# Performance work log

Hardware: AMD Instinct MI355X
Metric: run time of the kernel (lower is better)

## Reference

```python
import jax, jax.numpy as jnp
import numpy as np

B, C, T, H, K = 512, 64, 512, 128, 16
EPS_BN = 1e-5


def setup_inputs() -> dict:
    key = jax.random.key(0)
    ks = jax.random.split(key, 8)
    s = 0.05
    return {
        "x": jax.random.normal(ks[0], (B, C, T), jnp.float32),
        "conv1_w": jax.random.normal(ks[1], (H, C, 3), jnp.float32) * s,
        "conv1_b": jnp.zeros((H,), jnp.float32),
        "conv2_w": jax.random.normal(ks[2], (H, H, 3), jnp.float32) * s,
        "conv2_b": jnp.zeros((H,), jnp.float32),
        "bnt1_g": jnp.ones((H,), jnp.float32), "bnt1_b": jnp.zeros((H,), jnp.float32),
        "bnt2_g": jnp.ones((H,), jnp.float32), "bnt2_b": jnp.zeros((H,), jnp.float32),
        "W1": jax.random.normal(ks[3], (T, H), jnp.float32) * s, "b1": jnp.zeros((H,), jnp.float32),
        "g1": jnp.ones((H,), jnp.float32), "be1": jnp.zeros((H,), jnp.float32),
        "W2": jax.random.normal(ks[4], (H, H), jnp.float32) * s, "b2": jnp.zeros((H,), jnp.float32),
        "g2": jnp.ones((H,), jnp.float32), "be2": jnp.zeros((H,), jnp.float32),
        "W3": jax.random.normal(ks[5], (H, H), jnp.float32) * s, "b3": jnp.zeros((H,), jnp.float32),
        "g3": jnp.ones((H,), jnp.float32), "be3": jnp.zeros((H,), jnp.float32),
    }


def _bn_nc(z, g, b):
    # BatchNorm1d on (N, C) with batch statistics (training-mode normalization)
    m = z.mean(0)
    v = z.var(0)
    return (z - m) * jax.lax.rsqrt(v + EPS_BN) * g + b


def _bn_ncl(z, g, b):
    # BatchNorm1d on (N, C, L)
    m = z.mean((0, 2), keepdims=True)
    v = z.var((0, 2), keepdims=True)
    return (z - m) * jax.lax.rsqrt(v + EPS_BN) * g[None, :, None] + b[None, :, None]


def _conv1d(z, w, b):
    y = jax.lax.conv_general_dilated(z, w, (1,), "SAME",
                                     dimension_numbers=("NCH", "OIH", "NCH"))
    return y + b[None, :, None]


def _forward(x, conv1_w, conv1_b, conv2_w, conv2_b, bnt1_g, bnt1_b, bnt2_g, bnt2_b,
             W1, b1, g1, be1, W2, b2, g2, be2, W3, b3, g3, be3):
    # temporal branch: computed but unused in the output (faithful to the source)
    ht = jax.nn.relu(_bn_ncl(_conv1d(x, conv1_w, conv1_b), bnt1_g, bnt1_b))
    ht = jax.nn.relu(_bn_ncl(_conv1d(ht, conv2_w, conv2_b), bnt2_g, bnt2_b))

    # dynamic graph: cosine similarity averaged over batch, top-k neighbors per channel
    xn = x / jnp.maximum(jnp.linalg.norm(x, axis=2, keepdims=True), 1e-12)
    sim = jnp.einsum("bct,bdt->cd", xn, xn) / x.shape[0]  # (C, C)
    _, nbr = jax.lax.top_k(sim, K)                        # (C, K)
    src = jnp.repeat(jnp.arange(C), K)                    # (C*K,)
    dst = nbr.reshape(-1)                                 # (C*K,)
    offs = (jnp.arange(B) * C)[:, None]
    N = B * C
    sl = jnp.arange(N)
    # edge_index[0]=source node i, edge_index[1]=its top-k neighbor; plus GCN self-loops
    es = jnp.concatenate([(src[None, :] + offs).reshape(-1), sl])
    ed = jnp.concatenate([(dst[None, :] + offs).reshape(-1), sl])

    deg = jax.ops.segment_sum(jnp.ones(es.shape[0], x.dtype), ed, num_segments=N)
    dinv = jax.lax.rsqrt(deg)  # deg >= 1 due to self-loops
    enorm = dinv[es] * dinv[ed]

    def gcn(h, W, b):
        hw = h @ W
        return jax.ops.segment_sum(hw[es] * enorm[:, None], ed, num_segments=N) + b

    # source does permute(0,2,1).view(B*C, T): a flat reshape of the (B, T, C) tensor
    nodes = jnp.transpose(x, (0, 2, 1)).reshape(N, T)
    h = jax.nn.relu(_bn_nc(gcn(nodes, W1, b1), g1, be1))
    h = jax.nn.relu(_bn_nc(gcn(h, W2, b2), g2, be2))
    h = jax.nn.relu(_bn_nc(gcn(h, W3, b3), g3, be3))
    return h.reshape(B, C * H)


def reference(x, conv1_w, conv1_b, conv2_w, conv2_b, bnt1_g, bnt1_b, bnt2_g, bnt2_b,
              W1, b1, g1, be1, W2, b2, g2, be2, W3, b3, g3, be3):
    return _forward(x, conv1_w, conv1_b, conv2_w, conv2_b, bnt1_g, bnt1_b,
                    bnt2_g, bnt2_b, W1, b1, g1, be1, W2, b2, g2, be2,
                    W3, b3, g3, be3)
```

## Files before the change

### kernel.cpp

```cpp
#include <hip/hip_runtime.h>
#include <math.h>

#define B_  512
#define C_  64
#define T_  512
#define H_  128
#define N_  (B_*C_)

typedef unsigned int   uint_;
typedef unsigned short ushort_;
typedef unsigned long long ull_;

typedef __attribute__((ext_vector_type(8))) short bf8v;
typedef __attribute__((ext_vector_type(4))) float f4v;

#define OFF_SIMP   0u
#define OFF_Z2     0u
#define OFF_Z1     8388608u
#define OFF_Z3     16777216u
#define OFF_WT1    25165824u
#define OFF_WT2    25296896u
#define OFF_WT3    25329664u
#define OFF_MASKS  25362432u
#define OFF_MB     25395200u
#define OFF_SS1    25403392u
#define OFF_SS2    25404416u
#define OFF_SS3    25405440u
#define OFF_BNPART 25406464u
#define OFF_BNP2   25930752u

__device__ __forceinline__ ushort_ f2bf(float f) {
    uint_ u = __float_as_uint(f);
    u = (u + 0x7FFFu + ((u >> 16) & 1u)) >> 16;
    return (ushort_)u;
}
__device__ __forceinline__ float bf2f(ushort_ s) {
    return __uint_as_float(((uint_)s) << 16);
}

__global__ __launch_bounds__(256) void k_gram(const float* __restrict__ x,
                                              float* __restrict__ simpart)
{
    __shared__ ushort_ Xh[64 * 136];
    __shared__ ushort_ Xl[64 * 136];
    __shared__ float  gd[64];
    __shared__ double rn[64];

    const int b = blockIdx.x;
    const int t = threadIdx.x;
    const int w = t >> 6, l = t & 63;
    const int lr = l & 15, lg = l >> 4;
    const int r0 = (w >> 1) * 2, c0 = (w & 1) * 2;

    f4v acc[2][2];
#pragma unroll
    for (int i = 0; i < 2; ++i)
#pragma unroll
        for (int j = 0; j < 2; ++j) acc[i][j] = (f4v)0.f;

    const float* xb = x + (size_t)b * (C_ * T_);

    for (int j = 0; j < 4; ++j) {
#pragma unroll
        for (int it = 0; it < 8; ++it) {
            int i = t + 256 * it;
            int c = i >> 5, t4 = i & 31;
            float4 v = *(const float4*)&xb[(size_t)c * T_ + 128 * j + 4 * t4];
            ushort_ h0 = f2bf(v.x), h1 = f2bf(v.y), h2 = f2bf(v.z), h3 = f2bf(v.w);
            uint2 ph;
            ph.x = (uint_)h0 | ((uint_)h1 << 16);
            ph.y = (uint_)h2 | ((uint_)h3 << 16);
            float e0 = v.x - bf2f(h0), e1 = v.y - bf2f(h1);
            float e2 = v.z - bf2f(h2), e3 = v.w - bf2f(h3);
            uint2 pl;
            pl.x = (uint_)f2bf(e0) | ((uint_)f2bf(e1) << 16);
            pl.y = (uint_)f2bf(e2) | ((uint_)f2bf(e3) << 16);
            *(uint2*)&Xh[c * 136 + 4 * t4] = ph;
            *(uint2*)&Xl[c * 136 + 4 * t4] = pl;
        }
        __syncthreads();

#pragma unroll
        for (int s = 0; s < 4; ++s) {
            bf8v ah[2], al[2], bh[2], bl[2];
#pragma unroll
            for (int i = 0; i < 2; ++i) {
                ah[i] = *(const bf8v*)&Xh[(16 * (r0 + i) + lr) * 136 + 32 * s + 8 * lg];
                al[i] = *(const bf8v*)&Xl[(16 * (r0 + i) + lr) * 136 + 32 * s + 8 * lg];
                bh[i] = *(const bf8v*)&Xh[(16 * (c0 + i) + lr) * 136 + 32 * s + 8 * lg];
                bl[i] = *(const bf8v*)&Xl[(16 * (c0 + i) + lr) * 136 + 32 * s + 8 * lg];
            }
#pragma unroll
            for (int i = 0; i < 2; ++i)
#pragma unroll
                for (int jj = 0; jj < 2; ++jj) {
                    acc[i][jj] = __builtin_amdgcn_mfma_f32_16x16x32_bf16(ah[i], bh[jj], acc[i][jj], 0, 0, 0);
                    acc[i][jj] = __builtin_amdgcn_mfma_f32_16x16x32_bf16(ah[i], bl[jj], acc[i][jj], 0, 0, 0);
                    acc[i][jj] = __builtin_amdgcn_mfma_f32_16x16x32_bf16(al[i], bh[jj], acc[i][jj], 0, 0, 0);
                }
        }
        __syncthreads();
    }

    if (r0 == c0) {
#pragma unroll
        for (int d = 0; d < 2; ++d)
            if (lg == (lr >> 2)) gd[16 * (r0 + d) + lr] = acc[d][d][lr & 3];
    }
    __syncthreads();
    if (t < 64) rn[t] = 1.0 / fmax(sqrt((double)gd[t]), 1e-12);
    __syncthreads();

    float* sp = simpart + (size_t)b * 4096;
#pragma unroll
    for (int i = 0; i < 2; ++i)
#pragma unroll
        for (int jj = 0; jj < 2; ++jj)
#pragma unroll
            for (int reg = 0; reg < 4; ++reg) {
                int rc = 16 * (r0 + i) + 4 * lg + reg;
                int cc = 16 * (c0 + jj) + lr;
                sp[rc * 64 + cc] = (float)((double)acc[i][jj][reg] * rn[rc] * rn[cc]);
            }
}

__global__ __launch_bounds__(256) void k_simrank(const float* __restrict__ simpart,
                                                 ull_* __restrict__ masks)
{
    __shared__ double part[4][64];
    __shared__ double sd[64];
    const int c = blockIdx.x;
    const int t = threadIdx.x;
    const int d = t & 63, g = t >> 6;

    double a = 0.0;
    const float* sp = simpart + (size_t)c * 64 + d;
    for (int i = 0; i < 128; ++i)
        a += (double)sp[(size_t)(g + 4 * i) * 4096];
    part[g][d] = a;
    __syncthreads();

    if (t < 64) {
        double s = ((part[0][t] + part[1][t]) + part[2][t]) + part[3][t];
        sd[t] = s;
        int rank = 0;
#pragma unroll
        for (int dp = 0; dp < 64; ++dp) {
            double w = sd[dp];
            rank += (w > s || (w == s && dp < t)) ? 1 : 0;
        }
        ull_ m = __ballot(rank < 16);
        if (t == 0) masks[c] = m;
    }
}

__global__ __launch_bounds__(256) void k_mkM(const ull_* __restrict__ masks,
                                             ushort_* __restrict__ Mbout)
{
    __shared__ ull_  nbrm[64];
    __shared__ float dv[64];
    const int t = threadIdx.x;

    if (t < 64) {
        ull_ mask = masks[t];
        nbrm[t] = mask;
        int deg = 1;
#pragma unroll
        for (int d = 0; d < 64; ++d) {
            ull_ bal = __ballot((int)((mask >> d) & 1ull));
            if (t == d) deg += (int)__popcll(bal);
        }
        dv[t] = 1.0f / sqrtf((float)deg);
    }
    __syncthreads();

    const int d = t >> 2, q = t & 3;
    const float dvd = dv[d];
    uint_ buf[8];
#pragma unroll
    for (int p = 0; p < 8; ++p) {
        int c0 = 16 * q + 2 * p, c1 = c0 + 1;
        float w0 = (float)((int)((nbrm[c0] >> d) & 1ull) + (c0 == d ? 1 : 0));
        float w1 = (float)((int)((nbrm[c1] >> d) & 1ull) + (c1 == d ? 1 : 0));
        buf[p] = (uint_)f2bf(w0 * dv[c0] * dvd) |
                 ((uint_)f2bf(w1 * dv[c1] * dvd) << 16);
    }
    ushort_* dst = Mbout + d * 64 + 16 * q;
    uint4 v0 = {buf[0], buf[1], buf[2], buf[3]};
    uint4 v1 = {buf[4], buf[5], buf[6], buf[7]};
    *(uint4*)&dst[0] = v0;
    *(uint4*)&dst[8] = v1;
}

__global__ __launch_bounds__(256) void k_prepw(const float* __restrict__ W1,
    const float* __restrict__ W2, const float* __restrict__ W3,
    ushort_* __restrict__ Wt1, ushort_* __restrict__ Wt2, ushort_* __restrict__ Wt3)
{
    __shared__ float L[64 * 132];
    const int blk = blockIdx.x, t = threadIdx.x;

    if (blk < 8) {
        for (int it = 0; it < 8; ++it) {
            int i = t + 256 * it;
            int ri = i >> 5, f4 = i & 31;
            int m = ri >> 3, cr = ri & 7;
            *(float4*)&L[ri * 132 + 4 * f4] =
                *(const float4*)&W1[(size_t)(64 * m + 8 * blk + cr) * H_ + 4 * f4];
        }
        __syncthreads();
        int f = t >> 1, half = t & 1;
        uint_ buf[16];
#pragma unroll
        for (int jj = 0; jj < 16; ++jj) {
            int k0 = 32 * half + 2 * jj;
            int c0 = k0 >> 3, m0 = k0 & 7;
            int c1 = (k0 + 1) >> 3, m1 = (k0 + 1) & 7;
            buf[jj] = (uint_)f2bf(L[(m0 * 8 + c0) * 132 + f]) |
                      ((uint_)f2bf(L[(m1 * 8 + c1) * 132 + f]) << 16);
        }
        ushort_* dst = Wt1 + (size_t)f * 512 + 64 * blk + 32 * half;
#pragma unroll
        for (int q = 0; q < 4; ++q) {
            uint4 vv = {buf[4 * q], buf[4 * q + 1], buf[4 * q + 2], buf[4 * q + 3]};
            *(uint4*)&dst[8 * q] = vv;
        }
    } else {
        const float* W = (blk < 10) ? W2 : W3;
        ushort_*     O = (blk < 10) ? Wt2 : Wt3;
        int kb = (blk - 8) & 1;
        for (int it = 0; it < 8; ++it) {
            int i = t + 256 * it;
            int ri = i >> 5, f4 = i & 31;
            *(float4*)&L[ri * 132 + 4 * f4] =
                *(const float4*)&W[(size_t)(64 * kb + ri) * H_ + 4 * f4];
        }
        __syncthreads();
        int f = t >> 1, half = t & 1;
        uint_ buf[16];
#pragma unroll
        for (int jj = 0; jj < 16; ++jj) {
            int k0 = 32 * half + 2 * jj;
            buf[jj] = (uint_)f2bf(L[k0 * 132 + f]) |
                      ((uint_)f2bf(L[(k0 + 1) * 132 + f]) << 16);
        }
        ushort_* dst = O + (size_t)f * 128 + 64 * kb + 32 * half;
#pragma unroll
        for (int q = 0; q < 4; ++q) {
            uint4 vv = {buf[4 * q], buf[4 * q + 1], buf[4 * q + 2], buf[4 * q + 3]};
            *(uint4*)&dst[8 * q] = vv;
        }
    }
}

__device__ __forceinline__ void mfma_epilogue(char* smem, int b, int t,
    f4v acc[8], const float* __restrict__ bias, const ushort_* __restrict__ Mb,
    ushort_* __restrict__ Zout, float* __restrict__ bnpart)
{
    const int l = t & 63, w = t >> 6;
    const int lr = l & 15, lg = l >> 4;

    ushort_* Yt  = (ushort_*)smem;
    ushort_* Ml  = (ushort_*)(smem + 22528);
    ushort_* Zst = (ushort_*)(smem + 33792);

#pragma unroll
    for (int nt = 0; nt < 8; ++nt) {
        uint2 p;
        p.x = (uint_)f2bf(acc[nt][0]) | ((uint_)f2bf(acc[nt][1]) << 16);
        p.y = (uint_)f2bf(acc[nt][2]) | ((uint_)f2bf(acc[nt][3]) << 16);
        *(uint2*)&Yt[(16 * nt + lr) * 88 + 16 * w + 4 * lg] = p;
    }
#pragma unroll
    for (int it = 0; it < 2; ++it) {
        int i = t + 256 * it;
        int d = i >> 3, seg = i & 7;
        *(uint4*)&Ml[d * 88 + 8 * seg] = *(const uint4*)&Mb[d * 64 + 8 * seg];
    }
    __syncthreads();

    f4v z[8];
#pragma unroll
    for (int nt = 0; nt < 8; ++nt) z[nt] = (f4v)0.f;
#pragma unroll
    for (int cs = 0; cs < 2; ++cs) {
        bf8v mf = *(const bf8v*)&Ml[(16 * w + lr) * 88 + 32 * cs + 8 * lg];
#pragma unroll
        for (int nt = 0; nt < 8; ++nt) {
            bf8v yf = *(const bf8v*)&Yt[(16 * nt + lr) * 88 + 32 * cs + 8 * lg];
            z[nt] = __builtin_amdgcn_mfma_f32_16x16x32_bf16(mf, yf, z[nt], 0, 0, 0);
        }
    }

#pragma unroll
    for (int nt = 0; nt < 8; ++nt) {
        float bv = bias[16 * nt + lr];
#pragma unroll
        for (int reg = 0; reg < 4; ++reg)
            Zst[(16 * w + 4 * lg + reg) * 136 + 16 * nt + lr] = f2bf(z[nt][reg] + bv);
    }
    __syncthreads();

    if (t < 128) {
        float s = 0.f, s2 = 0.f;
        for (int r = 0; r < 64; ++r) {
            float v = bf2f(Zst[r * 136 + t]);
            s += v; s2 += v * v;
        }
        bnpart[b * 256 + t]       = s;
        bnpart[b * 256 + 128 + t] = s2;
    }
#pragma unroll
    for (int it = 0; it < 4; ++it) {
        int i = t + 256 * it;
        int r = i >> 4, seg = i & 15;
        *(uint4*)&Zout[((size_t)(b * 64 + r)) * 128 + 8 * seg] =
            *(const uint4*)&Zst[r * 136 + 8 * seg];
    }
}

__global__ __launch_bounds__(256) void k_mgemm1(const float* __restrict__ x,
    const ushort_* __restrict__ Wt, const float* __restrict__ bias,
    const ushort_* __restrict__ Mb, ushort_* __restrict__ Zout,
    float* __restrict__ bnpart)
{
    __shared__ __align__(16) char smem[51456];
    ushort_* Al = (ushort_*)smem;
    ushort_* Wl = (ushort_*)(smem + 16640);

    const int b = blockIdx.x;
    const int t = threadIdx.x;
    const int l = t & 63, w = t >> 6;
    const int lr = l & 15, lg = l >> 4;

    f4v acc[8];
#pragma unroll
    for (int nt = 0; nt < 8; ++nt) acc[nt] = (f4v)0.f;

    const float* xb = x + (size_t)b * (C_ * T_);

    for (int j = 0; j < 4; ++j) {
#pragma unroll
        for (int it = 0; it < 8; ++it) {
            int i = t + 256 * it;
            int cr = i >> 7, t4 = i & 127;
            float4 v = *(const float4*)&xb[(size_t)(16 * j + cr) * T_ + 4 * t4];
            uint2 p;
            p.x = (uint_)f2bf(v.x) | ((uint_)f2bf(v.y) << 16);
            p.y = (uint_)f2bf(v.z) | ((uint_)f2bf(v.w) << 16);
            *(uint2*)&Al[cr * 520 + 4 * t4] = p;
        }
#pragma unroll
        for (int it = 0; it < 8; ++it) {
            int i = t + 256 * it;
            int f = i >> 4, seg = i & 15;
            *(uint4*)&Wl[f * 136 + 8 * seg] =
                *(const uint4*)&Wt[(size_t)f * 512 + 128 * j + 8 * seg];
        }
        __syncthreads();
#pragma unroll
        for (int s = 0; s < 4; ++s) {
            bf8v af = *(const bf8v*)&Al[(4 * s + lg) * 520 + 128 * w + 8 * lr];
#pragma unroll
            for (int nt = 0; nt < 8; ++nt) {
                bf8v bfv = *(const bf8v*)&Wl[(16 * nt + lr) * 136 + 32 * s + 8 * lg];
                acc[nt] = __builtin_amdgcn_mfma_f32_16x16x32_bf16(af, bfv, acc[nt], 0, 0, 0);
            }
        }
        __syncthreads();
    }
    mfma_epilogue(smem, b, t, acc, bias, Mb, Zout, bnpart);
}

__global__ __launch_bounds__(256) void k_mgemm23(const ushort_* __restrict__ Zin,
    const float* __restrict__ ss, const ushort_* __restrict__ Wt,
    const float* __restrict__ bias, const ushort_* __restrict__ Mb,
    ushort_* __restrict__ Zout, float* __restrict__ bnpart)
{
    __shared__ __align__(16) char smem[52224];
    __shared__ float ssL[256];
    ushort_* Al = (ushort_*)smem;
    ushort_* Wl = (ushort_*)(smem + 17408);

    const int b = blockIdx.x;
    const int t = threadIdx.x;
    const int l = t & 63, w = t >> 6;
    const int lr = l & 15, lg = l >> 4;

    ssL[t] = ss[t];
    __syncthreads();

    f4v acc[8];
#pragma unroll
    for (int nt = 0; nt < 8; ++nt) acc[nt] = (f4v)0.f;

#pragma unroll
    for (int it = 0; it < 4; ++it) {
        int i = t + 256 * it;
        int r = i >> 4, seg = i & 15;
        uint4 v = *(const uint4*)&Zin[((size_t)(b * 64 + r)) * 128 + 8 * seg];
        uint_ w0[4] = {v.x, v.y, v.z, v.w};
        uint_ o[4];
#pragma unroll
        for (int p = 0; p < 4; ++p) {
            int f0 = 8 * seg + 2 * p;
            float z0 = bf2f((ushort_)(w0[p] & 0xFFFF));
            float z1 = bf2f((ushort_)(w0[p] >> 16));
            float h0 = fmaxf(fmaf(z0, ssL[f0],     ssL[128 + f0]),     0.f);
            float h1 = fmaxf(fmaf(z1, ssL[f0 + 1], ssL[128 + f0 + 1]), 0.f);
            o[p] = (uint_)f2bf(h0) | ((uint_)f2bf(h1) << 16);
        }
        uint4 ov = {o[0], o[1], o[2], o[3]};
        *(uint4*)&Al[r * 136 + 8 * seg] = ov;
    }
#pragma unroll
    for (int it = 0; it < 8; ++it) {
        int i = t + 256 * it;
        int f = i >> 4, seg = i & 15;
        *(uint4*)&Wl[f * 136 + 8 * seg] =
            *(const uint4*)&Wt[(size_t)f * 128 + 8 * seg];
    }
    __syncthreads();
#pragma unroll
    for (int s = 0; s < 4; ++s) {
        bf8v af = *(const bf8v*)&Al[(16 * w + lr) * 136 + 32 * s + 8 * lg];
#pragma unroll
        for (int nt = 0; nt < 8; ++nt) {
            bf8v bfv = *(const bf8v*)&Wl[(16 * nt + lr) * 136 + 32 * s + 8 * lg];
            acc[nt] = __builtin_amdgcn_mfma_f32_16x16x32_bf16(af, bfv, acc[nt], 0, 0, 0);
        }
    }
    __syncthreads();
    mfma_epilogue(smem, b, t, acc, bias, Mb, Zout, bnpart);
}

__global__ __launch_bounds__(256) void k_bnA(const float* __restrict__ bnpart,
                                             double* __restrict__ bnp2)
{
    const int t = threadIdx.x, g = blockIdx.x;
    double a = 0.0;
    for (int i = 0; i < 16; ++i)
        a += (double)bnpart[(size_t)(16 * g + i) * 256 + t];
    bnp2[(size_t)g * 256 + t] = a;
}

__global__ __launch_bounds__(256) void k_bnB(const double* __restrict__ bnp2,
    const float* __restrict__ g, const float* __restrict__ be, float* __restrict__ ss)
{
    __shared__ double sums[256];
    const int t = threadIdx.x;
    double a = 0.0;
    for (int q = 0; q < 32; ++q) a += bnp2[(size_t)q * 256 + t];
    sums[t] = a;
    __syncthreads();
    if (t < 128) {
        double s = sums[t], s2 = sums[128 + t];
        double mean = s * (1.0 / 32768.0);
        double var  = s2 * (1.0 / 32768.0) - mean * mean;
        double rstd = 1.0 / sqrt(var + 1e-5);
        float sc = (float)((double)g[t] * rstd);
        ss[t]       = sc;
        ss[128 + t] = (float)((double)be[t] - mean * (double)sc);
    }
}

__global__ __launch_bounds__(256) void k_out(const ushort_* __restrict__ Z,
    const float* __restrict__ ss, float* __restrict__ out)
{
    int i = blockIdx.x * 256 + threadIdx.x;
    int n = i >> 4, seg = i & 15;
    uint4 v = *(const uint4*)&Z[(size_t)n * 128 + 8 * seg];
    float4 sc0 = *(const float4*)&ss[8 * seg];
    float4 sc1 = *(const float4*)&ss[8 * seg + 4];
    float4 sh0 = *(const float4*)&ss[128 + 8 * seg];
    float4 sh1 = *(const float4*)&ss[128 + 8 * seg + 4];
    uint_ wv[4] = {v.x, v.y, v.z, v.w};
    float zz[8];
#pragma unroll
    for (int p = 0; p < 4; ++p) {
        zz[2 * p]     = bf2f((ushort_)(wv[p] & 0xFFFF));
        zz[2 * p + 1] = bf2f((ushort_)(wv[p] >> 16));
    }
    float4 o0, o1;
    o0.x = fmaxf(fmaf(zz[0], sc0.x, sh0.x), 0.f);
    o0.y = fmaxf(fmaf(zz[1], sc0.y, sh0.y), 0.f);
    o0.z = fmaxf(fmaf(zz[2], sc0.z, sh0.z), 0.f);
    o0.w = fmaxf(fmaf(zz[3], sc0.w, sh0.w), 0.f);
    o1.x = fmaxf(fmaf(zz[4], sc1.x, sh1.x), 0.f);
    o1.y = fmaxf(fmaf(zz[5], sc1.y, sh1.y), 0.f);
    o1.z = fmaxf(fmaf(zz[6], sc1.z, sh1.z), 0.f);
    o1.w = fmaxf(fmaf(zz[7], sc1.w, sh1.w), 0.f);
    *(float4*)&out[(size_t)n * 128 + 8 * seg]     = o0;
    *(float4*)&out[(size_t)n * 128 + 8 * seg + 4] = o1;
}

extern "C" void kernel_launch(void* const* d_in, const int* in_sizes, int n_in,
                              void* d_out, int out_size, void* d_ws, size_t ws_size,
                              hipStream_t stream)
{
    (void)in_sizes; (void)n_in; (void)out_size; (void)ws_size;

    const float* x   = (const float*)d_in[0];
    const float* W1  = (const float*)d_in[9];
    const float* b1  = (const float*)d_in[10];
    const float* g1  = (const float*)d_in[11];
    const float* be1 = (const float*)d_in[12];
    const float* W2  = (const float*)d_in[13];
    const float* b2  = (const float*)d_in[14];
    const float* g2  = (const float*)d_in[15];
    const float* be2 = (const float*)d_in[16];
    const float* W3  = (const float*)d_in[17];
    const float* b3  = (const float*)d_in[18];
    const float* g3  = (const float*)d_in[19];
    const float* be3 = (const float*)d_in[20];

    char* ws = (char*)d_ws;
    float*   simp   = (float*)(ws + OFF_SIMP);
    ull_*    masks  = (ull_*)(ws + OFF_MASKS);
    ushort_* Mb     = (ushort_*)(ws + OFF_MB);
    ushort_* Wt1    = (ushort_*)(ws + OFF_WT1);
    ushort_* Wt2    = (ushort_*)(ws + OFF_WT2);
    ushort_* Wt3    = (ushort_*)(ws + OFF_WT3);
    float*   ss1    = (float*)(ws + OFF_SS1);
    float*   ss2    = (float*)(ws + OFF_SS2);
    float*   ss3    = (float*)(ws + OFF_SS3);
    float*   bnpart = (float*)(ws + OFF_BNPART);
    double*  bnp2   = (double*)(ws + OFF_BNP2);
    ushort_* Z1     = (ushort_*)(ws + OFF_Z1);
    ushort_* Z2     = (ushort_*)(ws + OFF_Z2);
    ushort_* Z3     = (ushort_*)(ws + OFF_Z3);
    float*   out    = (float*)d_out;

    k_prepw<<<dim3(12), dim3(256), 0, stream>>>(W1, W2, W3, Wt1, Wt2, Wt3);
    k_gram<<<dim3(512), dim3(256), 0, stream>>>(x, simp);
    k_simrank<<<dim3(64), dim3(256), 0, stream>>>(simp, masks);
    k_mkM<<<dim3(1), dim3(256), 0, stream>>>(masks, Mb);

    k_mgemm1<<<dim3(512), dim3(256), 0, stream>>>(x, Wt1, b1, Mb, Z1, bnpart);
    k_bnA<<<dim3(32), dim3(256), 0, stream>>>(bnpart, bnp2);
    k_bnB<<<dim3(1), dim3(256), 0, stream>>>(bnp2, g1, be1, ss1);

    k_mgemm23<<<dim3(512), dim3(256), 0, stream>>>(Z1, ss1, Wt2, b2, Mb, Z2, bnpart);
    k_bnA<<<dim3(32), dim3(256), 0, stream>>>(bnpart, bnp2);
    k_bnB<<<dim3(1), dim3(256), 0, stream>>>(bnp2, g2, be2, ss2);

    k_mgemm23<<<dim3(512), dim3(256), 0, stream>>>(Z2, ss2, Wt3, b3, Mb, Z3, bnpart);
    k_bnA<<<dim3(32), dim3(256), 0, stream>>>(bnpart, bnp2);
    k_bnB<<<dim3(1), dim3(256), 0, stream>>>(bnp2, g3, be3, ss3);

    k_out<<<dim3(2048), dim3(256), 0, stream>>>(Z3, ss3, out);
}
```

Baseline: 107.1 us.

## Fold tiny setup kernels into neighbors to cut launch count

Merges weight preparation into the Gram kernel as extra blocks, and drops the single-block adjacency-matrix kernel by having each GEMM block rebuild the normalized adjacency from the masks. It also removes the BN finalize kernels by having every consumer block re-reduce the 32 partial sums and compute scale/shift itself. This removes five serial launches and their tail gaps, at the cost of redundant per-block reduction and mask work and more shared memory per block.

```diff
diff --git a/kernel.cpp b/kernel.cpp
--- a/kernel.cpp
+++ b/kernel.cpp
@@ -22,10 +22,6 @@
 #define OFF_WT2    25296896u
 #define OFF_WT3    25329664u
 #define OFF_MASKS  25362432u
-#define OFF_MB     25395200u
-#define OFF_SS1    25403392u
-#define OFF_SS2    25404416u
-#define OFF_SS3    25405440u
 #define OFF_BNPART 25406464u
 #define OFF_BNP2   25930752u
 
@@ -38,90 +34,182 @@
     return __uint_as_float(((uint_)s) << 16);
 }
 
-__global__ __launch_bounds__(256) void k_gram(const float* __restrict__ x,
-                                              float* __restrict__ simpart)
-{
-    __shared__ ushort_ Xh[64 * 136];
-    __shared__ ushort_ Xl[64 * 136];
+__device__ __forceinline__ void m_preamble_wave0(const ull_* __restrict__ masks,
+                                                 ull_* nbrmS, float* dvS, int t)
+{
+    if (t < 64) {
+        ull_ mask = masks[t];
+        nbrmS[t] = mask;
+        int deg = 1;
+#pragma unroll
+        for (int d = 0; d < 64; ++d) {
+            ull_ bal = __ballot((int)((mask >> d) & 1ull));
+            if (t == d) deg += (int)__popcll(bal);
+        }
+        dvS[t] = 1.0f / sqrtf((float)deg);
+    }
+}
+
+__device__ __forceinline__ void m_build(const ull_* nbrmS, const float* dvS,
+                                        int t, uint_ m8[8])
+{
+    const int d = t >> 2, q = t & 3;
+    const float dvd = dvS[d];
+#pragma unroll
+    for (int p = 0; p < 8; ++p) {
+        int c0 = 16 * q + 2 * p, c1 = c0 + 1;
+        float w0 = (float)((int)((nbrmS[c0] >> d) & 1ull) + (c0 == d ? 1 : 0));
+        float w1 = (float)((int)((nbrmS[c1] >> d) & 1ull) + (c1 == d ? 1 : 0));
+        m8[p] = (uint_)f2bf(w0 * dvS[c0] * dvd) |
+                ((uint_)f2bf(w1 * dvS[c1] * dvd) << 16);
+    }
+}
+
+__global__ __launch_bounds__(256) void k_gramw(const float* __restrict__ x,
+    float* __restrict__ simpart,
+    const float* __restrict__ W1, const float* __restrict__ W2,
+    const float* __restrict__ W3,
+    ushort_* __restrict__ Wt1, ushort_* __restrict__ Wt2, ushort_* __restrict__ Wt3)
+{
+    __shared__ __align__(16) char smem[35584];
     __shared__ float  gd[64];
     __shared__ double rn[64];
-
-    const int b = blockIdx.x;
+    const int blk = blockIdx.x;
     const int t = threadIdx.x;
-    const int w = t >> 6, l = t & 63;
-    const int lr = l & 15, lg = l >> 4;
-    const int r0 = (w >> 1) * 2, c0 = (w & 1) * 2;
-
-    f4v acc[2][2];
-#pragma unroll
-    for (int i = 0; i < 2; ++i)
-#pragma unroll
-        for (int j = 0; j < 2; ++j) acc[i][j] = (f4v)0.f;
-
-    const float* xb = x + (size_t)b * (C_ * T_);
-
-    for (int j = 0; j < 4; ++j) {
-#pragma unroll
-        for (int it = 0; it < 8; ++it) {
-            int i = t + 256 * it;
-            int c = i >> 5, t4 = i & 31;
-            float4 v = *(const float4*)&xb[(size_t)c * T_ + 128 * j + 4 * t4];
-            ushort_ h0 = f2bf(v.x), h1 = f2bf(v.y), h2 = f2bf(v.z), h3 = f2bf(v.w);
-            uint2 ph;
-            ph.x = (uint_)h0 | ((uint_)h1 << 16);
-            ph.y = (uint_)h2 | ((uint_)h3 << 16);
-            float e0 = v.x - bf2f(h0), e1 = v.y - bf2f(h1);
-            float e2 = v.z - bf2f(h2), e3 = v.w - bf2f(h3);
-            uint2 pl;
-            pl.x = (uint_)f2bf(e0) | ((uint_)f2bf(e1) << 16);
-            pl.y = (uint_)f2bf(e2) | ((uint_)f2bf(e3) << 16);
-            *(uint2*)&Xh[c * 136 + 4 * t4] = ph;
-            *(uint2*)&Xl[c * 136 + 4 * t4] = pl;
+
+    if (blk < 512) {
+        ushort_* Xh = (ushort_*)smem;
+        ushort_* Xl = (ushort_*)(smem + 17408);
+        const int b = blk;
+        const int w = t >> 6, l = t & 63;
+        const int lr = l & 15, lg = l >> 4;
+        const int r0 = (w >> 1) * 2, c0 = (w & 1) * 2;
+
+        f4v acc[2][2];
+#pragma unroll
+        for (int i = 0; i < 2; ++i)
+#pragma unroll
+            for (int j = 0; j < 2; ++j) acc[i][j] = (f4v)0.f;
+
+        const float* xb = x + (size_t)b * (C_ * T_);
+
+        for (int j = 0; j < 4; ++j) {
+#pragma unroll
+            for (int it = 0; it < 8; ++it) {
+                int i = t + 256 * it;
+                int c = i >> 5, t4 = i & 31;
+                float4 v = *(const float4*)&xb[(size_t)c * T_ + 128 * j + 4 * t4];
+                ushort_ h0 = f2bf(v.x), h1 = f2bf(v.y), h2 = f2bf(v.z), h3 = f2bf(v.w);
+                uint2 ph;
+                ph.x = (uint_)h0 | ((uint_)h1 << 16);
+                ph.y = (uint_)h2 | ((uint_)h3 << 16);
+                float e0 = v.x - bf2f(h0), e1 = v.y - bf2f(h1);
+                float e2 = v.z - bf2f(h2), e3 = v.w - bf2f(h3);
+                uint2 pl;
+                pl.x = (uint_)f2bf(e0) | ((uint_)f2bf(e1) << 16);
+                pl.y = (uint_)f2bf(e2) | ((uint_)f2bf(e3) << 16);
+                *(uint2*)&Xh[c * 136 + 4 * t4] = ph;
+                *(uint2*)&Xl[c * 136 + 4 * t4] = pl;
+            }
+            __syncthreads();
+
+#pragma unroll
+            for (int s = 0; s < 4; ++s) {
+                bf8v ah[2], al[2], bh[2], bl[2];
+#pragma unroll
+                for (int i = 0; i < 2; ++i) {
+                    ah[i] = *(const bf8v*)&Xh[(16 * (r0 + i) + lr) * 136 + 32 * s + 8 * lg];
+                    al[i] = *(const bf8v*)&Xl[(16 * (r0 + i) + lr) * 136 + 32 * s + 8 * lg];
+                    bh[i] = *(const bf8v*)&Xh[(16 * (c0 + i) + lr) * 136 + 32 * s + 8 * lg];
+                    bl[i] = *(const bf8v*)&Xl[(16 * (c0 + i) + lr) * 136 + 32 * s + 8 * lg];
+                }
+#pragma unroll
+                for (int i = 0; i < 2; ++i)
+#pragma unroll
+                    for (int jj = 0; jj < 2; ++jj) {
+                        acc[i][jj] = __builtin_amdgcn_mfma_f32_16x16x32_bf16(ah[i], bh[jj], acc[i][jj], 0, 0, 0);
+                        acc[i][jj] = __builtin_amdgcn_mfma_f32_16x16x32_bf16(ah[i], bl[jj], acc[i][jj], 0, 0, 0);
+                        acc[i][jj] = __builtin_amdgcn_mfma_f32_16x16x32_bf16(al[i], bh[jj], acc[i][jj], 0, 0, 0);
+                    }
+            }
+            __syncthreads();
+        }
+
+        if (r0 == c0) {
+#pragma unroll
+            for (int d = 0; d < 2; ++d)
+                if (lg == (lr >> 2)) gd[16 * (r0 + d) + lr] = acc[d][d][lr & 3];
         }
         __syncthreads();
-
-#pragma unroll
-        for (int s = 0; s < 4; ++s) {
-            bf8v ah[2], al[2], bh[2], bl[2];
-#pragma unroll
-            for (int i = 0; i < 2; ++i) {
-                ah[i] = *(const bf8v*)&Xh[(16 * (r0 + i) + lr) * 136 + 32 * s + 8 * lg];
-                al[i] = *(const bf8v*)&Xl[(16 * (r0 + i) + lr) * 136 + 32 * s + 8 * lg];
-                bh[i] = *(const bf8v*)&Xh[(16 * (c0 + i) + lr) * 136 + 32 * s + 8 * lg];
-                bl[i] = *(const bf8v*)&Xl[(16 * (c0 + i) + lr) * 136 + 32 * s + 8 * lg];
-            }
-#pragma unroll
-            for (int i = 0; i < 2; ++i)
-#pragma unroll
-                for (int jj = 0; jj < 2; ++jj) {
-                    acc[i][jj] = __builtin_amdgcn_mfma_f32_16x16x32_bf16(ah[i], bh[jj], acc[i][jj], 0, 0, 0);
-                    acc[i][jj] = __builtin_amdgcn_mfma_f32_16x16x32_bf16(ah[i], bl[jj], acc[i][jj], 0, 0, 0);
-                    acc[i][jj] = __builtin_amdgcn_mfma_f32_16x16x32_bf16(al[i], bh[jj], acc[i][jj], 0, 0, 0);
+        if (t < 64) rn[t] = 1.0 / fmax(sqrt((double)gd[t]), 1e-12);
+        __syncthreads();
+
+        float* sp = simpart + (size_t)b * 4096;
+#pragma unroll
+        for (int i = 0; i < 2; ++i)
+#pragma unroll
+            for (int jj = 0; jj < 2; ++jj)
+#pragma unroll
+                for (int reg = 0; reg < 4; ++reg) {
+                    int rc = 16 * (r0 + i) + 4 * lg + reg;
+                    int cc = 16 * (c0 + jj) + lr;
+                    sp[rc * 64 + cc] = (float)((double)acc[i][jj][reg] * rn[rc] * rn[cc]);
                 }
-        }
-        __syncthreads();
-    }
-
-    if (r0 == c0) {
-#pragma unroll
-        for (int d = 0; d < 2; ++d)
-            if (lg == (lr >> 2)) gd[16 * (r0 + d) + lr] = acc[d][d][lr & 3];
-    }
-    __syncthreads();
-    if (t < 64) rn[t] = 1.0 / fmax(sqrt((double)gd[t]), 1e-12);
-    __syncthreads();
-
-    float* sp = simpart + (size_t)b * 4096;
-#pragma unroll
-    for (int i = 0; i < 2; ++i)
-#pragma unroll
-        for (int jj = 0; jj < 2; ++jj)
-#pragma unroll
-            for (int reg = 0; reg < 4; ++reg) {
-                int rc = 16 * (r0 + i) + 4 * lg + reg;
-                int cc = 16 * (c0 + jj) + lr;
-                sp[rc * 64 + cc] = (float)((double)acc[i][jj][reg] * rn[rc] * rn[cc]);
-            }
+    } else {
+        float* L = (float*)smem;
+        const int pblk = blk - 512;
+        if (pblk < 8) {
+            for (int it = 0; it < 8; ++it) {
+                int i = t + 256 * it;
+                int ri = i >> 5, f4 = i & 31;
+                int m = ri >> 3, cr = ri & 7;
+                *(float4*)&L[ri * 132 + 4 * f4] =
+                    *(const float4*)&W1[(size_t)(64 * m + 8 * pblk + cr) * H_ + 4 * f4];
+            }
+            __syncthreads();
+            int f = t >> 1, half = t & 1;
+            uint_ buf[16];
+#pragma unroll
+            for (int jj = 0; jj < 16; ++jj) {
+                int k0 = 32 * half + 2 * jj;
+                int c0 = k0 >> 3, m0 = k0 & 7;
+                int c1 = (k0 + 1) >> 3, m1 = (k0 + 1) & 7;
+                buf[jj] = (uint_)f2bf(L[(m0 * 8 + c0) * 132 + f]) |
+                          ((uint_)f2bf(L[(m1 * 8 + c1) * 132 + f]) << 16);
+            }
+            ushort_* dst = Wt1 + (size_t)f * 512 + 64 * pblk + 32 * half;
+#pragma unroll
+            for (int q = 0; q < 4; ++q) {
+                uint4 vv = {buf[4 * q], buf[4 * q + 1], buf[4 * q + 2], buf[4 * q + 3]};
+                *(uint4*)&dst[8 * q] = vv;
+            }
+        } else {
+            const float* W = (pblk < 10) ? W2 : W3;
+            ushort_*     O = (pblk < 10) ? Wt2 : Wt3;
+            int kb = (pblk - 8) & 1;
+            for (int it = 0; it < 8; ++it) {
+                int i = t + 256 * it;
+                int ri = i >> 5, f4 = i & 31;
+                *(float4*)&L[ri * 132 + 4 * f4] =
+                    *(const float4*)&W[(size_t)(64 * kb + ri) * H_ + 4 * f4];
+            }
+            __syncthreads();
+            int f = t >> 1, half = t & 1;
+            uint_ buf[16];
+#pragma unroll
+            for (int jj = 0; jj < 16; ++jj) {
+                int k0 = 32 * half + 2 * jj;
+                buf[jj] = (uint_)f2bf(L[k0 * 132 + f]) |
+                          ((uint_)f2bf(L[(k0 + 1) * 132 + f]) << 16);
+            }
+            ushort_* dst = O + (size_t)f * 128 + 64 * kb + 32 * half;
+#pragma unroll
+            for (int q = 0; q < 4; ++q) {
+                uint4 vv = {buf[4 * q], buf[4 * q + 1], buf[4 * q + 2], buf[4 * q + 3]};
+                *(uint4*)&dst[8 * q] = vv;
+            }
+        }
+    }
 }
 
 __global__ __launch_bounds__(256) void k_simrank(const float* __restrict__ simpart,
@@ -154,106 +242,8 @@
     }
 }
 
-__global__ __launch_bounds__(256) void k_mkM(const ull_* __restrict__ masks,
-                                             ushort_* __restrict__ Mbout)
-{
-    __shared__ ull_  nbrm[64];
-    __shared__ float dv[64];
-    const int t = threadIdx.x;
-
-    if (t < 64) {
-        ull_ mask = masks[t];
-        nbrm[t] = mask;
-        int deg = 1;
-#pragma unroll
-        for (int d = 0; d < 64; ++d) {
-            ull_ bal = __ballot((int)((mask >> d) & 1ull));
-            if (t == d) deg += (int)__popcll(bal);
-        }
-        dv[t] = 1.0f / sqrtf((float)deg);
-    }
-    __syncthreads();
-
-    const int d = t >> 2, q = t & 3;
-    const float dvd = dv[d];
-    uint_ buf[8];
-#pragma unroll
-    for (int p = 0; p < 8; ++p) {
-        int c0 = 16 * q + 2 * p, c1 = c0 + 1;
-        float w0 = (float)((int)((nbrm[c0] >> d) & 1ull) + (c0 == d ? 1 : 0));
-        float w1 = (float)((int)((nbrm[c1] >> d) & 1ull) + (c1 == d ? 1 : 0));
-        buf[p] = (uint_)f2bf(w0 * dv[c0] * dvd) |
-                 ((uint_)f2bf(w1 * dv[c1] * dvd) << 16);
-    }
-    ushort_* dst = Mbout + d * 64 + 16 * q;
-    uint4 v0 = {buf[0], buf[1], buf[2], buf[3]};
-    uint4 v1 = {buf[4], buf[5], buf[6], buf[7]};
-    *(uint4*)&dst[0] = v0;
-    *(uint4*)&dst[8] = v1;
-}
-
-__global__ __launch_bounds__(256) void k_prepw(const float* __restrict__ W1,
-    const float* __restrict__ W2, const float* __restrict__ W3,
-    ushort_* __restrict__ Wt1, ushort_* __restrict__ Wt2, ushort_* __restrict__ Wt3)
-{
-    __shared__ float L[64 * 132];
-    const int blk = blockIdx.x, t = threadIdx.x;
-
-    if (blk < 8) {
-        for (int it = 0; it < 8; ++it) {
-            int i = t + 256 * it;
-            int ri = i >> 5, f4 = i & 31;
-            int m = ri >> 3, cr = ri & 7;
-            *(float4*)&L[ri * 132 + 4 * f4] =
-                *(const float4*)&W1[(size_t)(64 * m + 8 * blk + cr) * H_ + 4 * f4];
-        }
-        __syncthreads();
-        int f = t >> 1, half = t & 1;
-        uint_ buf[16];
-#pragma unroll
-        for (int jj = 0; jj < 16; ++jj) {
-            int k0 = 32 * half + 2 * jj;
-            int c0 = k0 >> 3, m0 = k0 & 7;
-            int c1 = (k0 + 1) >> 3, m1 = (k0 + 1) & 7;
-            buf[jj] = (uint_)f2bf(L[(m0 * 8 + c0) * 132 + f]) |
-                      ((uint_)f2bf(L[(m1 * 8 + c1) * 132 + f]) << 16);
-        }
-        ushort_* dst = Wt1 + (size_t)f * 512 + 64 * blk + 32 * half;
-#pragma unroll
-        for (int q = 0; q < 4; ++q) {
-            uint4 vv = {buf[4 * q], buf[4 * q + 1], buf[4 * q + 2], buf[4 * q + 3]};
-            *(uint4*)&dst[8 * q] = vv;
-        }
-    } else {
-        const float* W = (blk < 10) ? W2 : W3;
-        ushort_*     O = (blk < 10) ? Wt2 : Wt3;
-        int kb = (blk - 8) & 1;
-        for (int it = 0; it < 8; ++it) {
-            int i = t + 256 * it;
-            int ri = i >> 5, f4 = i & 31;
-            *(float4*)&L[ri * 132 + 4 * f4] =
-                *(const float4*)&W[(size_t)(64 * kb + ri) * H_ + 4 * f4];
-        }
-        __syncthreads();
-        int f = t >> 1, half = t & 1;
-        uint_ buf[16];
-#pragma unroll
-        for (int jj = 0; jj < 16; ++jj) {
-            int k0 = 32 * half + 2 * jj;
-            buf[jj] = (uint_)f2bf(L[k0 * 132 + f]) |
-                      ((uint_)f2bf(L[(k0 + 1) * 132 + f]) << 16);
-        }
-        ushort_* dst = O + (size_t)f * 128 + 64 * kb + 32 * half;
-#pragma unroll
-        for (int q = 0; q < 4; ++q) {
-            uint4 vv = {buf[4 * q], buf[4 * q + 1], buf[4 * q + 2], buf[4 * q + 3]};
-            *(uint4*)&dst[8 * q] = vv;
-        }
-    }
-}
-
 __device__ __forceinline__ void mfma_epilogue(char* smem, int b, int t,
-    f4v acc[8], const float* __restrict__ bias, const ushort_* __restrict__ Mb,
+    f4v acc[8], const float* __restrict__ bias, const uint_ m8[8],
     ushort_* __restrict__ Zout, float* __restrict__ bnpart)
 {
     const int l = t & 63, w = t >> 6;
@@ -270,11 +260,12 @@
         p.y = (uint_)f2bf(acc[nt][2]) | ((uint_)f2bf(acc[nt][3]) << 16);
         *(uint2*)&Yt[(16 * nt + lr) * 88 + 16 * w + 4 * lg] = p;
     }
-#pragma unroll
-    for (int it = 0; it < 2; ++it) {
-        int i = t + 256 * it;
-        int d = i >> 3, seg = i & 7;
-        *(uint4*)&Ml[d * 88 + 8 * seg] = *(const uint4*)&Mb[d * 64 + 8 * seg];
+    {
+        const int d = t >> 2, q = t & 3;
+        uint4 v0 = {m8[0], m8[1], m8[2], m8[3]};
+        uint4 v1 = {m8[4], m8[5], m8[6], m8[7]};
+        *(uint4*)&Ml[d * 88 + 16 * q]     = v0;
+        *(uint4*)&Ml[d * 88 + 16 * q + 8] = v1;
     }
     __syncthreads();
 
@@ -320,10 +311,12 @@
 
 __global__ __launch_bounds__(256) void k_mgemm1(const float* __restrict__ x,
     const ushort_* __restrict__ Wt, const float* __restrict__ bias,
-    const ushort_* __restrict__ Mb, ushort_* __restrict__ Zout,
+    const ull_* __restrict__ masks, ushort_* __restrict__ Zout,
     float* __restrict__ bnpart)
 {
     __shared__ __align__(16) char smem[51456];
+    __shared__ ull_  nbrmS[64];
+    __shared__ float dvS[64];
     ushort_* Al = (ushort_*)smem;
     ushort_* Wl = (ushort_*)(smem + 16640);
 
@@ -331,6 +324,8 @@
     const int t = threadIdx.x;
     const int l = t & 63, w = t >> 6;
     const int lr = l & 15, lg = l >> 4;
+
+    m_preamble_wave0(masks, nbrmS, dvS, t);
 
     f4v acc[8];
 #pragma unroll
@@ -368,16 +363,22 @@
         }
         __syncthreads();
     }
-    mfma_epilogue(smem, b, t, acc, bias, Mb, Zout, bnpart);
+
+    uint_ m8[8];
+    m_build(nbrmS, dvS, t, m8);
+    mfma_epilogue(smem, b, t, acc, bias, m8, Zout, bnpart);
 }
 
 __global__ __launch_bounds__(256) void k_mgemm23(const ushort_* __restrict__ Zin,
-    const float* __restrict__ ss, const ushort_* __restrict__ Wt,
-    const float* __restrict__ bias, const ushort_* __restrict__ Mb,
+    const double* __restrict__ bnp2, const float* __restrict__ g,
+    const float* __restrict__ be, const ushort_* __restrict__ Wt,
+    const float* __restrict__ bias, const ull_* __restrict__ masks,
     ushort_* __restrict__ Zout, float* __restrict__ bnpart)
 {
     __shared__ __align__(16) char smem[52224];
     __shared__ float ssL[256];
+    __shared__ ull_  nbrmS[64];
+    __shared__ float dvS[64];
     ushort_* Al = (ushort_*)smem;
     ushort_* Wl = (ushort_*)(smem + 17408);
 
@@ -386,8 +387,24 @@
     const int l = t & 63, w = t >> 6;
     const int lr = l & 15, lg = l >> 4;
 
-    ssL[t] = ss[t];
-    __syncthreads();
+    {
+        double* sumsL = (double*)smem;
+        double a = 0.0;
+        for (int q = 0; q < 32; ++q) a += bnp2[(size_t)q * 256 + t];
+        sumsL[t] = a;
+        m_preamble_wave0(masks, nbrmS, dvS, t);
+        __syncthreads();
+        if (t < 128) {
+            double s = sumsL[t], s2 = sumsL[128 + t];
+            double mean = s * (1.0 / 32768.0);
+            double var  = s2 * (1.0 / 32768.0) - mean * mean;
+            double rstd = 1.0 / sqrt(var + 1e-5);
+            float sc = (float)((double)g[t] * rstd);
+            ssL[t]       = sc;
+            ssL[128 + t] = (float)((double)be[t] - mean * (double)sc);
+        }
+        __syncthreads();
+    }
 
     f4v acc[8];
 #pragma unroll
@@ -430,7 +447,10 @@
         }
     }
     __syncthreads();
-    mfma_epilogue(smem, b, t, acc, bias, Mb, Zout, bnpart);
+
+    uint_ m8[8];
+    m_build(nbrmS, dvS, t, m8);
+    mfma_epilogue(smem, b, t, acc, bias, m8, Zout, bnpart);
 }
 
 __global__ __launch_bounds__(256) void k_bnA(const float* __restrict__ bnpart,
@@ -443,54 +463,49 @@
     bnp2[(size_t)g * 256 + t] = a;
 }
 
-__global__ __launch_bounds__(256) void k_bnB(const double* __restrict__ bnp2,
-    const float* __restrict__ g, const float* __restrict__ be, float* __restrict__ ss)
-{
-    __shared__ double sums[256];
+__global__ __launch_bounds__(256) void k_out(const ushort_* __restrict__ Z,
+    const double* __restrict__ bnp2, const float* __restrict__ g,
+    const float* __restrict__ be, float* __restrict__ out)
+{
+    __shared__ double sumsL[256];
+    __shared__ float  ssL[256];
+    const int b = blockIdx.x;
     const int t = threadIdx.x;
+
     double a = 0.0;
     for (int q = 0; q < 32; ++q) a += bnp2[(size_t)q * 256 + t];
-    sums[t] = a;
+    sumsL[t] = a;
     __syncthreads();
     if (t < 128) {
-        double s = sums[t], s2 = sums[128 + t];
+        double s = sumsL[t], s2 = sumsL[128 + t];
         double mean = s * (1.0 / 32768.0);
         double var  = s2 * (1.0 / 32768.0) - mean * mean;
         double rstd = 1.0 / sqrt(var + 1e-5);
         float sc = (float)((double)g[t] * rstd);
-        ss[t]       = sc;
-        ss[128 + t] = (float)((double)be[t] - mean * (double)sc);
-    }
-}
-
-__global__ __launch_bounds__(256) void k_out(const ushort_* __restrict__ Z,
-    const float* __restrict__ ss, float* __restrict__ out)
-{
-    int i = blockIdx.x * 256 + threadIdx.x;
-    int n = i >> 4, seg = i & 15;
-    uint4 v = *(const uint4*)&Z[(size_t)n * 128 + 8 * seg];
-    float4 sc0 = *(const float4*)&ss[8 * seg];
-    float4 sc1 = *(const float4*)&ss[8 * seg + 4];
-    float4 sh0 = *(const float4*)&ss[128 + 8 * seg];
-    float4 sh1 = *(const float4*)&ss[128 + 8 * seg + 4];
-    uint_ wv[4] = {v.x, v.y, v.z, v.w};
-    float zz[8];
-#pragma unroll
-    for (int p = 0; p < 4; ++p) {
-        zz[2 * p]     = bf2f((ushort_)(wv[p] & 0xFFFF));
-        zz[2 * p + 1] = bf2f((ushort_)(wv[p] >> 16));
-    }
-    float4 o0, o1;
-    o0.x = fmaxf(fmaf(zz[0], sc0.x, sh0.x), 0.f);
-    o0.y = fmaxf(fmaf(zz[1], sc0.y, sh0.y), 0.f);
-    o0.z = fmaxf(fmaf(zz[2], sc0.z, sh0.z), 0.f);
-    o0.w = fmaxf(fmaf(zz[3], sc0.w, sh0.w), 0.f);
-    o1.x = fmaxf(fmaf(zz[4], sc1.x, sh1.x), 0.f);
-    o1.y = fmaxf(fmaf(zz[5], sc1.y, sh1.y), 0.f);
-    o1.z = fmaxf(fmaf(zz[6], sc1.z, sh1.z), 0.f);
-    o1.w = fmaxf(fmaf(zz[7], sc1.w, sh1.w), 0.f);
-    *(float4*)&out[(size_t)n * 128 + 8 * seg]     = o0;
-    *(float4*)&out[(size_t)n * 128 + 8 * seg + 4] = o1;
+        ssL[t]       = sc;
+        ssL[128 + t] = (float)((double)be[t] - mean * (double)sc);
+    }
+    __syncthreads();
+
+    const size_t base = (size_t)b * 64 * 128;
+#pragma unroll
+    for (int it = 0; it < 8; ++it) {
+        int i = t + 256 * it;
+        int r = i >> 5, s = i & 31;
+        uint2 v = *(const uint2*)&Z[base + (size_t)r * 128 + 4 * s];
+        float4 sc = *(const float4*)&ssL[4 * s];
+        float4 sh = *(const float4*)&ssL[128 + 4 * s];
+        float z0 = bf2f((ushort_)(v.x & 0xFFFF));
+        float z1 = bf2f((ushort_)(v.x >> 16));
+        float z2 = bf2f((ushort_)(v.y & 0xFFFF));
+        float z3 = bf2f((ushort_)(v.y >> 16));
+        float4 o;
+        o.x = fmaxf(fmaf(z0, sc.x, sh.x), 0.f);
+        o.y = fmaxf(fmaf(z1, sc.y, sh.y), 0.f);
+        o.z = fmaxf(fmaf(z2, sc.z, sh.z), 0.f);
+        o.w = fmaxf(fmaf(z3, sc.w, sh.w), 0.f);
+        *(float4*)&out[base + (size_t)r * 128 + 4 * s] = o;
+    }
 }
 
 extern "C" void kernel_launch(void* const* d_in, const int* in_sizes, int n_in,
@@ -516,13 +531,9 @@
     char* ws = (char*)d_ws;
     float*   simp   = (float*)(ws + OFF_SIMP);
     ull_*    masks  = (ull_*)(ws + OFF_MASKS);
-    ushort_* Mb     = (ushort_*)(ws + OFF_MB);
     ushort_* Wt1    = (ushort_*)(ws + OFF_WT1);
     ushort_* Wt2    = (ushort_*)(ws + OFF_WT2);
     ushort_* Wt3    = (ushort_*)(ws + OFF_WT3);
-    float*   ss1    = (float*)(ws + OFF_SS1);
-    float*   ss2    = (float*)(ws + OFF_SS2);
-    float*   ss3    = (float*)(ws + OFF_SS3);
     float*   bnpart = (float*)(ws + OFF_BNPART);
     double*  bnp2   = (double*)(ws + OFF_BNP2);
     ushort_* Z1     = (ushort_*)(ws + OFF_Z1);
@@ -530,22 +541,17 @@
     ushort_* Z3     = (ushort_*)(ws + OFF_Z3);
     float*   out    = (float*)d_out;
 
-    k_prepw<<<dim3(12), dim3(256), 0, stream>>>(W1, W2, W3, Wt1, Wt2, Wt3);
-    k_gram<<<dim3(512), dim3(256), 0, stream>>>(x, simp);
+    k_gramw<<<dim3(524), dim3(256), 0, stream>>>(x, simp, W1, W2, W3, Wt1, Wt2, Wt3);
     k_simrank<<<dim3(64), dim3(256), 0, stream>>>(simp, masks);
-    k_mkM<<<dim3(1), dim3(256), 0, stream>>>(masks, Mb);
-
-    k_mgemm1<<<dim3(512), dim3(256), 0, stream>>>(x, Wt1, b1, Mb, Z1, bnpart);
+
+    k_mgemm1<<<dim3(512), dim3(256), 0, stream>>>(x, Wt1, b1, masks, Z1, bnpart);
     k_bnA<<<dim3(32), dim3(256), 0, stream>>>(bnpart, bnp2);
-    k_bnB<<<dim3(1), dim3(256), 0, stream>>>(bnp2, g1, be1, ss1);
-
-    k_mgemm23<<<dim3(512), dim3(256), 0, stream>>>(Z1, ss1, Wt2, b2, Mb, Z2, bnpart);
+
+    k_mgemm23<<<dim3(512), dim3(256), 0, stream>>>(Z1, bnp2, g1, be1, Wt2, b2, masks, Z2, bnpart);
     k_bnA<<<dim3(32), dim3(256), 0, stream>>>(bnpart, bnp2);
-    k_bnB<<<dim3(1), dim3(256), 0, stream>>>(bnp2, g2, be2, ss2);
-
-    k_mgemm23<<<dim3(512), dim3(256), 0, stream>>>(Z2, ss2, Wt3, b3, Mb, Z3, bnpart);
+
+    k_mgemm23<<<dim3(512), dim3(256), 0, stream>>>(Z2, bnp2, g2, be2, Wt3, b3, masks, Z3, bnpart);
     k_bnA<<<dim3(32), dim3(256), 0, stream>>>(bnpart, bnp2);
-    k_bnB<<<dim3(1), dim3(256), 0, stream>>>(bnp2, g3, be3, ss3);
-
-    k_out<<<dim3(2048), dim3(256), 0, stream>>>(Z3, ss3, out);
-}
+
+    k_out<<<dim3(512), dim3(256), 0, stream>>>(Z3, bnp2, g3, be3, out);
+}
```

Result: faster. 99.92 us (-6.7%).
